# Optimization experiments

Measured on AMD Instinct MI355X. Metric: run time of the kernel, lower is better.

## Reference

```python
import jax, jax.numpy as jnp
import numpy as np

B = 512
IN_DIM = 128
H2 = 512   # 2 * hidden_dim
OUT_DIM = 25


def setup_inputs() -> dict:
    key = jax.random.key(0)
    ks = jax.random.split(key, 12)
    s_in = 1.0 / np.sqrt(IN_DIM)
    s_h = 1.0 / np.sqrt(H2)
    return {
        "x": jax.random.normal(ks[0], (B, IN_DIM), dtype=jnp.float32),
        "na": 4,
        "W_in": jax.random.uniform(ks[1], (H2, IN_DIM), jnp.float32, -s_in, s_in),
        "b_in": jax.random.uniform(ks[2], (H2,), jnp.float32, -s_in, s_in),
        "Aq": jax.random.normal(ks[3], (H2, H2), dtype=jnp.float32),
        "Bq": jax.random.normal(ks[4], (H2,), dtype=jnp.float32),
        "Ak": jax.random.normal(ks[5], (H2, H2), dtype=jnp.float32),
        "Bk": jax.random.normal(ks[6], (H2,), dtype=jnp.float32),
        "Av": jax.random.normal(ks[7], (H2, H2), dtype=jnp.float32),
        "Bv": jax.random.normal(ks[8], (H2,), dtype=jnp.float32),
        "W_out": jax.random.uniform(ks[9], (OUT_DIM, H2), jnp.float32, -s_h, s_h),
        "b_out": jax.random.uniform(ks[10], (OUT_DIM,), jnp.float32, -s_h, s_h),
    }


def reference(x, na, W_in, b_in, Aq, Bq, Ak, Bk, Av, Bv, W_out, b_out):
    silu = jax.nn.silu
    h = silu(x @ W_in.T + b_in)                 # [B, 2H]  mlp_in
    # repeat+bmm is just a shared linear map per sample
    Q = silu(h @ Aq.T + Bq)                     # [B, 2H]
    K = silu(h @ Ak.T + Bk)                     # [B, 2H]
    V = silu(h @ Av.T + Bv)                     # [B, 2H]
    # scores = Q outer K, softmax over last dim, then matvec with V
    scores = Q[:, :, None] * K[:, None, :]      # [B, 2H, 2H]
    attn = jax.nn.softmax(scores, axis=2)
    ctx = silu(jnp.einsum('bij,bj->bi', attn, V))  # [B, 2H]
    y = silu(ctx @ W_out.T + b_out)             # [B, 25]  mlp_out

    y2 = y * y
    m11 = y2[:, 0:5].sum(1)                     # [B]
    m12 = y2[:, 5:10].sum(1)
    m21 = y2[:, 10:15].sum(1)
    m22 = y2[:, 15:20].sum(1)
    mpp = y2[:, 20:25].sum(1)                   # [B]

    eye2 = jnp.eye(2, dtype=y.dtype)
    blk = lambda m: m[:, None, None] * eye2     # [B, 2, 2] diag block
    M = jnp.concatenate(
        [jnp.concatenate([blk(m11), blk(m21)], axis=1),
         jnp.concatenate([blk(m12), blk(m22)], axis=1)],
        axis=2)                                  # [B, 4, 4]
    q = y[:, :4]                                # [B, 4]
    quad = jnp.einsum('bi,bij,bj->b', q, M, q)  # [B]
    return (quad + mpp)[:, None]                # [B, 1]
```

## Files before the change

### kernel.cpp

```cpp
#include <hip/hip_runtime.h>

#define NB   512
#define IND  128
#define H    512
#define OUTD 25

__device__ __forceinline__ float silu_f(float v) {
    return v / (1.0f + __expf(-v));
}

__device__ __forceinline__ float dot4(float4 a, float4 b) {
    return fmaf(a.x, b.x, fmaf(a.y, b.y, fmaf(a.z, b.z, a.w * b.w)));
}

__global__ __launch_bounds__(256) void k_hin(const float* __restrict__ x,
                                             const float* __restrict__ Win,
                                             const float* __restrict__ bin,
                                             float* __restrict__ h) {
    const int b0  = blockIdx.x * 2;
    const int col = blockIdx.y * 256 + threadIdx.x;

    const float4* w  = (const float4*)(Win + (size_t)col * IND);
    const float4* x0 = (const float4*)(x + (size_t)b0 * IND);
    const float4* x1 = (const float4*)(x + (size_t)(b0 + 1) * IND);

    float a0 = 0.0f, a1 = 0.0f;
#pragma unroll 8
    for (int k4 = 0; k4 < IND / 4; ++k4) {
        const float4 wv = w[k4];
        a0 += dot4(wv, x0[k4]);
        a1 += dot4(wv, x1[k4]);
    }
    const float bi = bin[col];
    h[(size_t)b0 * H + col]       = silu_f(a0 + bi);
    h[(size_t)(b0 + 1) * H + col] = silu_f(a1 + bi);
}

__global__ __launch_bounds__(128) void k_qkv(const float* __restrict__ h,
                                             const float* __restrict__ Aq,
                                             const float* __restrict__ Bq,
                                             const float* __restrict__ Ak,
                                             const float* __restrict__ Bk,
                                             const float* __restrict__ Av,
                                             const float* __restrict__ Bv,
                                             float* __restrict__ qkv) {
    const int b0 = blockIdx.x * 8;
    const int r  = blockIdx.y * 128 + threadIdx.x;
    const int m  = blockIdx.z;

    const float* A  = (m == 0) ? Aq : (m == 1) ? Ak : Av;
    const float* Bb = (m == 0) ? Bq : (m == 1) ? Bk : Bv;

    const float4* w = (const float4*)(A + (size_t)r * H);

    float acc[8] = {};
#pragma unroll 2
    for (int k4 = 0; k4 < H / 4; ++k4) {
        const float4 wv = w[k4];
#pragma unroll
        for (int bb = 0; bb < 8; ++bb) {
            const float4 hv = *(const float4*)(h + (size_t)(b0 + bb) * H + k4 * 4);
            acc[bb] += dot4(wv, hv);
        }
    }
    const float bias = Bb[r];
#pragma unroll
    for (int bb = 0; bb < 8; ++bb) {
        qkv[(size_t)m * NB * H + (size_t)(b0 + bb) * H + r] = silu_f(acc[bb] + bias);
    }
}

__global__ __launch_bounds__(512) void k_attn(const float* __restrict__ qkv,
                                              float* __restrict__ ctx) {
    __shared__ float wmx[8], wmn[8];

    const int b = blockIdx.x;
    const int t = threadIdx.x;

    const float* Q = qkv + (size_t)b * H;
    const float* K = qkv + 1 * (size_t)NB * H + (size_t)b * H;
    const float* V = qkv + 2 * (size_t)NB * H + (size_t)b * H;

    const float kv = K[t];
    float mx = kv, mn = kv;
#pragma unroll
    for (int o = 32; o > 0; o >>= 1) {
        mx = fmaxf(mx, __shfl_xor(mx, o, 64));
        mn = fminf(mn, __shfl_xor(mn, o, 64));
    }
    const int lane = t & 63, w = t >> 6;
    if (lane == 0) { wmx[w] = mx; wmn[w] = mn; }
    __syncthreads();

    float gmx = wmx[0], gmn = wmn[0];
#pragma unroll
    for (int i = 1; i < 8; ++i) {
        gmx = fmaxf(gmx, wmx[i]);
        gmn = fminf(gmn, wmn[i]);
    }

    const float s  = Q[t];
    const float m  = (s >= 0.0f) ? s * gmx : s * gmn;
    const float nm = -m;

    float den = 0.0f, num = 0.0f;
    const float4* K4p = (const float4*)K;
    const float4* V4p = (const float4*)V;
#pragma unroll 4
    for (int j4 = 0; j4 < H / 4; ++j4) {
        const float4 kj = K4p[j4];
        const float4 vj = V4p[j4];
        const float e0 = __expf(fmaf(s, kj.x, nm));
        const float e1 = __expf(fmaf(s, kj.y, nm));
        const float e2 = __expf(fmaf(s, kj.z, nm));
        const float e3 = __expf(fmaf(s, kj.w, nm));
        den += (e0 + e1) + (e2 + e3);
        num = fmaf(e0, vj.x, num);
        num = fmaf(e1, vj.y, num);
        num = fmaf(e2, vj.z, num);
        num = fmaf(e3, vj.w, num);
    }
    ctx[(size_t)b * H + t] = silu_f(num / den);
}

__global__ __launch_bounds__(256) void k_out(const float* __restrict__ ctx,
                                             const float* __restrict__ Wout,
                                             const float* __restrict__ bout,
                                             float* __restrict__ out) {
    __shared__ float cs[H];
    __shared__ float part[OUTD][8];
    __shared__ float yrow[OUTD];

    const int b = blockIdx.x;
    const int t = threadIdx.x;

    cs[t]       = ctx[(size_t)b * H + t];
    cs[t + 256] = ctx[(size_t)b * H + t + 256];
    __syncthreads();

    if (t < OUTD * 8) {
        const int o = t >> 3, p = t & 7;
        const float4* w = (const float4*)(Wout + (size_t)o * H + p * 64);
        const float4* c = (const float4*)(cs + p * 64);
        float a = 0.0f;
#pragma unroll
        for (int k = 0; k < 16; ++k) a += dot4(w[k], c[k]);
        part[o][p] = a;
    }
    __syncthreads();

    if (t < OUTD) {
        float a = bout[t];
#pragma unroll
        for (int p = 0; p < 8; ++p) a += part[t][p];
        yrow[t] = silu_f(a);
    }
    __syncthreads();

    if (t == 0) {
        float ms[5];
#pragma unroll
        for (int g = 0; g < 5; ++g) {
            float a = 0.0f;
#pragma unroll
            for (int k = 0; k < 5; ++k) {
                const float yv = yrow[g * 5 + k];
                a = fmaf(yv, yv, a);
            }
            ms[g] = a;
        }
        const float m11 = ms[0], m12 = ms[1], m21 = ms[2], m22 = ms[3], mpp = ms[4];
        const float q0 = yrow[0], q1 = yrow[1], q2 = yrow[2], q3 = yrow[3];
        const float quad = m11 * (q0 * q0 + q1 * q1)
                         + (m12 + m21) * (q0 * q2 + q1 * q3)
                         + m22 * (q2 * q2 + q3 * q3);
        out[b] = quad + mpp;
    }
}

extern "C" void kernel_launch(void* const* d_in, const int* in_sizes, int n_in,
                              void* d_out, int out_size, void* d_ws, size_t ws_size,
                              hipStream_t stream) {
    const float* x    = (const float*)d_in[0];
    const float* Win  = (const float*)d_in[2];
    const float* bin  = (const float*)d_in[3];
    const float* Aq   = (const float*)d_in[4];
    const float* Bq   = (const float*)d_in[5];
    const float* Ak   = (const float*)d_in[6];
    const float* Bk   = (const float*)d_in[7];
    const float* Av   = (const float*)d_in[8];
    const float* Bv   = (const float*)d_in[9];
    const float* Wout = (const float*)d_in[10];
    const float* bout = (const float*)d_in[11];

    float* out = (float*)d_out;
    float* ws  = (float*)d_ws;

    float* h   = ws;
    float* qkv = ws + (size_t)NB * H;
    float* ctx = ws + 4 * (size_t)NB * H;

    k_hin <<<dim3(NB / 2, 2),    dim3(256), 0, stream>>>(x, Win, bin, h);
    k_qkv <<<dim3(NB / 8, 4, 3), dim3(128), 0, stream>>>(h, Aq, Bq, Ak, Bk, Av, Bv, qkv);
    k_attn<<<dim3(NB),           dim3(512), 0, stream>>>(qkv, ctx);
    k_out <<<dim3(NB),           dim3(256), 0, stream>>>(ctx, Wout, bout, out);
}
```

Baseline: 145.8 us.

## Transpose hidden activations for coalesced QKV GEMV and fuse attention with output MLP

k_hin now writes h transposed (hidden-major), so k_qkv can read coalesced float4 batch vectors while each wave broadcasts one weight row. k_qkv is remapped to one wave per output row with four batch samples per lane. The attention and output kernels are merged so ctx stays in shared memory, which removes one launch and a global round trip. In exchange, qkv stores are strided by H across lanes and the weight row is read as scalar loads, which may cost bandwidth.

```diff
diff --git a/kernel.cpp b/kernel.cpp
--- a/kernel.cpp
+++ b/kernel.cpp
@@ -16,27 +16,26 @@
 __global__ __launch_bounds__(256) void k_hin(const float* __restrict__ x,
                                              const float* __restrict__ Win,
                                              const float* __restrict__ bin,
-                                             float* __restrict__ h) {
-    const int b0  = blockIdx.x * 2;
-    const int col = blockIdx.y * 256 + threadIdx.x;
-
-    const float4* w  = (const float4*)(Win + (size_t)col * IND);
-    const float4* x0 = (const float4*)(x + (size_t)b0 * IND);
-    const float4* x1 = (const float4*)(x + (size_t)(b0 + 1) * IND);
+                                             float* __restrict__ hT) {
+    const int b  = blockIdx.x * 256 + threadIdx.x;
+    const int j0 = blockIdx.y * 2;
+
+    const float4* xb = (const float4*)(x + (size_t)b * IND);
+    const float4* w0 = (const float4*)(Win + (size_t)j0 * IND);
+    const float4* w1 = (const float4*)(Win + (size_t)(j0 + 1) * IND);
 
     float a0 = 0.0f, a1 = 0.0f;
 #pragma unroll 8
     for (int k4 = 0; k4 < IND / 4; ++k4) {
-        const float4 wv = w[k4];
-        a0 += dot4(wv, x0[k4]);
-        a1 += dot4(wv, x1[k4]);
-    }
-    const float bi = bin[col];
-    h[(size_t)b0 * H + col]       = silu_f(a0 + bi);
-    h[(size_t)(b0 + 1) * H + col] = silu_f(a1 + bi);
-}
-
-__global__ __launch_bounds__(128) void k_qkv(const float* __restrict__ h,
+        const float4 xv = xb[k4];
+        a0 += dot4(w0[k4], xv);
+        a1 += dot4(w1[k4], xv);
+    }
+    hT[(size_t)j0 * NB + b]       = silu_f(a0 + bin[j0]);
+    hT[(size_t)(j0 + 1) * NB + b] = silu_f(a1 + bin[j0 + 1]);
+}
+
+__global__ __launch_bounds__(512) void k_qkv(const float* __restrict__ hT,
                                              const float* __restrict__ Aq,
                                              const float* __restrict__ Bq,
                                              const float* __restrict__ Ak,
@@ -44,35 +43,56 @@
                                              const float* __restrict__ Av,
                                              const float* __restrict__ Bv,
                                              float* __restrict__ qkv) {
-    const int b0 = blockIdx.x * 8;
-    const int r  = blockIdx.y * 128 + threadIdx.x;
-    const int m  = blockIdx.z;
-
-    const float* A  = (m == 0) ? Aq : (m == 1) ? Ak : Av;
-    const float* Bb = (m == 0) ? Bq : (m == 1) ? Bk : Bv;
-
-    const float4* w = (const float4*)(A + (size_t)r * H);
-
-    float acc[8] = {};
-#pragma unroll 2
-    for (int k4 = 0; k4 < H / 4; ++k4) {
-        const float4 wv = w[k4];
-#pragma unroll
-        for (int bb = 0; bb < 8; ++bb) {
-            const float4 hv = *(const float4*)(h + (size_t)(b0 + bb) * H + k4 * 4);
-            acc[bb] += dot4(wv, hv);
-        }
-    }
-    const float bias = Bb[r];
-#pragma unroll
-    for (int bb = 0; bb < 8; ++bb) {
-        qkv[(size_t)m * NB * H + (size_t)(b0 + bb) * H + r] = silu_f(acc[bb] + bias);
-    }
-}
-
-__global__ __launch_bounds__(512) void k_attn(const float* __restrict__ qkv,
-                                              float* __restrict__ ctx) {
+    const int t    = threadIdx.x;
+    const int wave = t >> 6;
+    const int lane = t & 63;
+
+    const int r = blockIdx.x * 8 + wave;
+    const int b = blockIdx.y * 256 + lane * 4;
+    const int m = blockIdx.z;
+
+    const float* A   = (m == 0) ? Aq : (m == 1) ? Ak : Av;
+    const float* Bm  = (m == 0) ? Bq : (m == 1) ? Bk : Bv;
+    const float* arow = A + (size_t)r * H;
+
+    float4 accA = {0.f, 0.f, 0.f, 0.f};
+    float4 accB = {0.f, 0.f, 0.f, 0.f};
+#pragma unroll 4
+    for (int k = 0; k < H; k += 2) {
+        const float4 h0 = *(const float4*)(hT + (size_t)k * NB + b);
+        const float4 h1 = *(const float4*)(hT + (size_t)(k + 1) * NB + b);
+        const float a0 = arow[k];
+        const float a1 = arow[k + 1];
+        accA.x = fmaf(a0, h0.x, accA.x);
+        accA.y = fmaf(a0, h0.y, accA.y);
+        accA.z = fmaf(a0, h0.z, accA.z);
+        accA.w = fmaf(a0, h0.w, accA.w);
+        accB.x = fmaf(a1, h1.x, accB.x);
+        accB.y = fmaf(a1, h1.y, accB.y);
+        accB.z = fmaf(a1, h1.z, accB.z);
+        accB.w = fmaf(a1, h1.w, accB.w);
+    }
+    const float bias = Bm[r];
+    const float o0 = silu_f(accA.x + accB.x + bias);
+    const float o1 = silu_f(accA.y + accB.y + bias);
+    const float o2 = silu_f(accA.z + accB.z + bias);
+    const float o3 = silu_f(accA.w + accB.w + bias);
+
+    float* dst = qkv + (size_t)m * NB * H + (size_t)b * H + r;
+    dst[0 * H] = o0;
+    dst[1 * H] = o1;
+    dst[2 * H] = o2;
+    dst[3 * H] = o3;
+}
+
+__global__ __launch_bounds__(512) void k_attn_out(const float* __restrict__ qkv,
+                                                  const float* __restrict__ Wout,
+                                                  const float* __restrict__ bout,
+                                                  float* __restrict__ out) {
     __shared__ float wmx[8], wmn[8];
+    __shared__ float cs[H];
+    __shared__ float part[OUTD][8];
+    __shared__ float yrow[OUTD];
 
     const int b = blockIdx.x;
     const int t = threadIdx.x;
@@ -120,31 +140,16 @@
         num = fmaf(e2, vj.z, num);
         num = fmaf(e3, vj.w, num);
     }
-    ctx[(size_t)b * H + t] = silu_f(num / den);
-}
-
-__global__ __launch_bounds__(256) void k_out(const float* __restrict__ ctx,
-                                             const float* __restrict__ Wout,
-                                             const float* __restrict__ bout,
-                                             float* __restrict__ out) {
-    __shared__ float cs[H];
-    __shared__ float part[OUTD][8];
-    __shared__ float yrow[OUTD];
-
-    const int b = blockIdx.x;
-    const int t = threadIdx.x;
-
-    cs[t]       = ctx[(size_t)b * H + t];
-    cs[t + 256] = ctx[(size_t)b * H + t + 256];
+    cs[t] = silu_f(num / den);
     __syncthreads();
 
     if (t < OUTD * 8) {
         const int o = t >> 3, p = t & 7;
-        const float4* w = (const float4*)(Wout + (size_t)o * H + p * 64);
-        const float4* c = (const float4*)(cs + p * 64);
+        const float4* wv = (const float4*)(Wout + (size_t)o * H + p * 64);
+        const float4* c  = (const float4*)(cs + p * 64);
         float a = 0.0f;
 #pragma unroll
-        for (int k = 0; k < 16; ++k) a += dot4(w[k], c[k]);
+        for (int k = 0; k < 16; ++k) a += dot4(wv[k], c[k]);
         part[o][p] = a;
     }
     __syncthreads();
@@ -196,12 +201,10 @@
     float* out = (float*)d_out;
     float* ws  = (float*)d_ws;
 
-    float* h   = ws;
+    float* hT  = ws;
     float* qkv = ws + (size_t)NB * H;
-    float* ctx = ws + 4 * (size_t)NB * H;
-
-    k_hin <<<dim3(NB / 2, 2),    dim3(256), 0, stream>>>(x, Win, bin, h);
-    k_qkv <<<dim3(NB / 8, 4, 3), dim3(128), 0, stream>>>(h, Aq, Bq, Ak, Bk, Av, Bv, qkv);
-    k_attn<<<dim3(NB),           dim3(512), 0, stream>>>(qkv, ctx);
-    k_out <<<dim3(NB),           dim3(256), 0, stream>>>(ctx, Wout, bout, out);
-}
+
+    k_hin     <<<dim3(2, 256),   dim3(256), 0, stream>>>(x, Win, bin, hT);
+    k_qkv     <<<dim3(64, 2, 3), dim3(512), 0, stream>>>(hT, Aq, Bq, Ak, Bk, Av, Bv, qkv);
+    k_attn_out<<<dim3(NB),       dim3(512), 0, stream>>>(qkv, Wout, bout, out);
+}
```

New measurement: 189.1 us. 29.7% more time.
